# Kernel tuning notes

Hardware: AMD Instinct MI355X
Metric: run time of the kernel (lower is better)

Reference implementation:

```python
import jax, jax.numpy as jnp
import numpy as np

N, M_CODES, Z_DIM = 4096, 4096, 1024


def setup_inputs() -> dict:
    key = jax.random.key(0)
    k1, k2 = jax.random.split(key)
    z = jax.random.normal(k1, (N, Z_DIM), dtype=jnp.float32)
    e = jax.random.normal(k2, (M_CODES, Z_DIM), dtype=jnp.float32)
    return {"z": z, "e": e}


def reference(z, e):
    # Squared pairwise L2 distances [N, M] via GEMM expansion:
    # ||z_i - e_j||^2 = ||z_i||^2 + ||e_j||^2 - 2 z_i . e_j
    z_sq = jnp.sum(z * z, axis=1)               # [N]
    e_sq = jnp.sum(e * e, axis=1)               # [M]
    cross = jnp.einsum('nd,md->nm', z, e)       # [N, M]
    dist = z_sq[:, None] + e_sq[None, :] - 2.0 * cross  # [N, M]
    # min over dim 0 (over data points N) -> per-code nearest distance [M]
    loss = jnp.mean(jnp.min(dist, axis=0))
    return loss
```

## Files before the change

### kernel.cpp

```cpp
#include <hip/hip_runtime.h>
#include <hip/hip_bf16.h>
#include <stdint.h>

#define N_PTS   4096
#define M_CODES 4096
#define ZDIM    1024
#define BM 128
#define BN 128
#define BK 32

typedef __attribute__((ext_vector_type(8))) short bf16x8;
typedef __attribute__((ext_vector_type(4))) float f32x4;

__device__ __forceinline__ unsigned short f2bf(float f) {
    __hip_bfloat16 h = __float2bfloat16(f);
    return *reinterpret_cast<unsigned short*>(&h);
}

__device__ __forceinline__ unsigned enc_f32(float f) {
    unsigned u = __float_as_uint(f);
    return (u & 0x80000000u) ? ~u : (u | 0x80000000u);
}
__device__ __forceinline__ float dec_f32(unsigned e) {
    unsigned u = (e & 0x80000000u) ? (e ^ 0x80000000u) : ~e;
    return __uint_as_float(u);
}

__global__ __launch_bounds__(256) void prep_kernel(
    const float* __restrict__ z, const float* __restrict__ e,
    unsigned short* __restrict__ zb, unsigned short* __restrict__ eb,
    float* __restrict__ zsq, float* __restrict__ esq,
    unsigned* __restrict__ min_enc) {
    const int t = threadIdx.x;
    const int b = blockIdx.x;
    if (b < 16) min_enc[b * 256 + t] = 0xFFFFFFFFu;

    const int w = t >> 6, lane = t & 63;
    const bool is_z = b < 512;
    #pragma unroll
    for (int r2 = 0; r2 < 2; r2++) {
        const int rr = (b & 511) * 8 + w * 2 + r2;
        const float4* s4 =
            reinterpret_cast<const float4*>((is_z ? z : e) + (size_t)rr * ZDIM);
        ushort4* d4 =
            reinterpret_cast<ushort4*>((is_z ? zb : eb) + (size_t)rr * ZDIM);
        float4 v0 = s4[lane], v1 = s4[64 + lane], v2 = s4[128 + lane],
               v3 = s4[192 + lane];
        ushort4 o0, o1, o2, o3;
        o0.x = f2bf(v0.x); o0.y = f2bf(v0.y); o0.z = f2bf(v0.z); o0.w = f2bf(v0.w);
        o1.x = f2bf(v1.x); o1.y = f2bf(v1.y); o1.z = f2bf(v1.z); o1.w = f2bf(v1.w);
        o2.x = f2bf(v2.x); o2.y = f2bf(v2.y); o2.z = f2bf(v2.z); o2.w = f2bf(v2.w);
        o3.x = f2bf(v3.x); o3.y = f2bf(v3.y); o3.z = f2bf(v3.z); o3.w = f2bf(v3.w);
        d4[lane] = o0; d4[64 + lane] = o1; d4[128 + lane] = o2; d4[192 + lane] = o3;
        float s = v0.x * v0.x + v0.y * v0.y + v0.z * v0.z + v0.w * v0.w
                + v1.x * v1.x + v1.y * v1.y + v1.z * v1.z + v1.w * v1.w
                + v2.x * v2.x + v2.y * v2.y + v2.z * v2.z + v2.w * v2.w
                + v3.x * v3.x + v3.y * v3.y + v3.z * v3.z + v3.w * v3.w;
        #pragma unroll
        for (int off = 1; off < 64; off <<= 1) s += __shfl_xor(s, off, 64);
        if (lane == 0) {
            if (is_z) zsq[rr] = s; else esq[rr] = s;
        }
    }
}

__global__ __launch_bounds__(256) void gemm_min_kernel(
    const unsigned short* __restrict__ zb, const unsigned short* __restrict__ eb,
    const float* __restrict__ zsq, unsigned* __restrict__ min_enc) {
    __shared__ __align__(16) unsigned short As[2 * BM * BK];
    __shared__ __align__(16) unsigned short Bs[2 * BN * BK];
    __shared__ float zsq_s[BM];

    const int t = threadIdx.x;
    const int bx = blockIdx.x;
    const int by = blockIdx.y;
    const int lane = t & 63;
    const int w = t >> 6;
    const int wm = w >> 1, wn = w & 1;
    const int lrow = lane & 15;
    const int q = lane >> 4;

    if (t < BM) zsq_s[t] = zsq[by * BM + t];

    f32x4 acc[4][4];
    #pragma unroll
    for (int i = 0; i < 4; i++)
        #pragma unroll
        for (int j = 0; j < 4; j++) acc[i][j] = (f32x4){0.f, 0.f, 0.f, 0.f};

    const int row0 = (t * 16) >> 6;
    const int kel0 = ((t * 16) & 63) >> 1;
    const int lds_b0 = w * 512;
    const size_t a_base = (size_t)(by * BM) * ZDIM;
    const size_t b_base = (size_t)(bx * BN) * ZDIM;

    for (int k0 = 0; k0 < ZDIM; k0 += 2 * BK) {
        #pragma unroll
        for (int s = 0; s < 2; s++) {
            const unsigned short* ga0 =
                zb + a_base + (size_t)row0 * ZDIM + k0 + s * BK + kel0;
            const unsigned short* gb0 =
                eb + b_base + (size_t)row0 * ZDIM + k0 + s * BK + kel0;
            __builtin_amdgcn_global_load_lds(
                (const __attribute__((address_space(1))) void*)ga0,
                (__attribute__((address_space(3))) void*)(As + s * 4096 + lds_b0),
                16, 0, 0);
            __builtin_amdgcn_global_load_lds(
                (const __attribute__((address_space(1))) void*)(ga0 + (size_t)64 * ZDIM),
                (__attribute__((address_space(3))) void*)(As + s * 4096 + 2048 + lds_b0),
                16, 0, 0);
            __builtin_amdgcn_global_load_lds(
                (const __attribute__((address_space(1))) void*)gb0,
                (__attribute__((address_space(3))) void*)(Bs + s * 4096 + lds_b0),
                16, 0, 0);
            __builtin_amdgcn_global_load_lds(
                (const __attribute__((address_space(1))) void*)(gb0 + (size_t)64 * ZDIM),
                (__attribute__((address_space(3))) void*)(Bs + s * 4096 + 2048 + lds_b0),
                16, 0, 0);
        }
        __syncthreads();

        #pragma unroll
        for (int s = 0; s < 2; s++) {
            bf16x8 a[4], bb[4];
            #pragma unroll
            for (int am = 0; am < 4; am++)
                a[am] = *(const bf16x8*)(As + s * 4096 +
                                         (wm * 64 + am * 16 + lrow) * BK + q * 8);
            #pragma unroll
            for (int an = 0; an < 4; an++)
                bb[an] = *(const bf16x8*)(Bs + s * 4096 +
                                          (wn * 64 + an * 16 + lrow) * BK + q * 8);
            #pragma unroll
            for (int am = 0; am < 4; am++)
                #pragma unroll
                for (int an = 0; an < 4; an++)
                    acc[am][an] = __builtin_amdgcn_mfma_f32_16x16x32_bf16(
                        a[am], bb[an], acc[am][an], 0, 0, 0);
        }
        __syncthreads();
    }

    #pragma unroll
    for (int an = 0; an < 4; an++) {
        float v = 3.4e38f;
        #pragma unroll
        for (int am = 0; am < 4; am++) {
            const int rbase = wm * 64 + am * 16 + q * 4;
            f32x4 c = acc[am][an];
            v = fminf(v, zsq_s[rbase + 0] - 2.f * c[0]);
            v = fminf(v, zsq_s[rbase + 1] - 2.f * c[1]);
            v = fminf(v, zsq_s[rbase + 2] - 2.f * c[2]);
            v = fminf(v, zsq_s[rbase + 3] - 2.f * c[3]);
        }
        v = fminf(v, __shfl_xor(v, 16, 64));
        v = fminf(v, __shfl_xor(v, 32, 64));
        if (q == 0) {
            const int col = bx * BN + wn * 64 + an * 16 + lrow;
            atomicMin(&min_enc[col], enc_f32(v));
        }
    }
}

__global__ __launch_bounds__(256) void finalize_kernel(
    const unsigned* __restrict__ min_enc, const float* __restrict__ esq,
    float* __restrict__ out) {
    const int t = threadIdx.x;
    float s = 0.f;
    #pragma unroll
    for (int i = 0; i < M_CODES / 256; i++) {
        const int j = i * 256 + t;
        s += dec_f32(min_enc[j]) + esq[j];
    }
    #pragma unroll
    for (int off = 1; off < 64; off <<= 1) s += __shfl_xor(s, off, 64);
    __shared__ float red[4];
    if ((t & 63) == 0) red[t >> 6] = s;
    __syncthreads();
    if (t == 0) out[0] = (red[0] + red[1] + red[2] + red[3]) * (1.f / M_CODES);
}

extern "C" void kernel_launch(void* const* d_in, const int* in_sizes, int n_in,
                              void* d_out, int out_size, void* d_ws, size_t ws_size,
                              hipStream_t stream) {
    (void)in_sizes; (void)n_in; (void)out_size; (void)ws_size;
    const float* z = (const float*)d_in[0];
    const float* e = (const float*)d_in[1];
    char* ws = (char*)d_ws;
    unsigned short* zb = (unsigned short*)ws;
    unsigned short* eb = (unsigned short*)(ws + ((size_t)8 << 20));
    float* zsq = (float*)(ws + ((size_t)16 << 20));
    float* esq = (float*)(ws + ((size_t)16 << 20) + 16384);
    unsigned* min_enc = (unsigned*)(ws + ((size_t)16 << 20) + 32768);

    prep_kernel<<<dim3(1024), dim3(256), 0, stream>>>(
        z, e, zb, eb, zsq, esq, min_enc);
    gemm_min_kernel<<<dim3(M_CODES / BN, N_PTS / BM), dim3(256), 0, stream>>>(
        zb, eb, zsq, min_enc);
    finalize_kernel<<<dim3(1), dim3(256), 0, stream>>>(min_enc, esq, (float*)d_out);
}
```

Baseline: 117.1 us.

## Pre-swizzle bf16 operands into MFMA fragment layout and use 2-wave 128x128 tiles

The prep kernel now stages 16 rows in LDS and writes the bf16 copies of z and e in a tiled layout, grouped by 16-row panel and 8-element k-group. The GEMM can then fetch each fragment with contiguous lane*8 LDS reads, avoiding strided row access and bank conflicts. The GEMM block shrinks to 128 threads (2 waves), each wave computing 64x128 with 32 accumulators, and loads a 64-wide k slab per iteration. Column minima are combined across waves in LDS before a single atomicMin per column. The trade-off is higher register pressure and fewer waves per block, which may reduce latency hiding.

```diff
diff --git a/kernel.cpp b/kernel.cpp
--- a/kernel.cpp
+++ b/kernel.cpp
@@ -5,9 +5,7 @@
 #define N_PTS   4096
 #define M_CODES 4096
 #define ZDIM    1024
-#define BM 128
-#define BN 128
-#define BK 32
+#define KG      (ZDIM / 8)
 
 typedef __attribute__((ext_vector_type(8))) short bf16x8;
 typedef __attribute__((ext_vector_type(4))) float f32x4;
@@ -16,7 +14,6 @@
     __hip_bfloat16 h = __float2bfloat16(f);
     return *reinterpret_cast<unsigned short*>(&h);
 }
-
 __device__ __forceinline__ unsigned enc_f32(float f) {
     unsigned u = __float_as_uint(f);
     return (u & 0x80000000u) ? ~u : (u | 0x80000000u);
@@ -26,115 +23,109 @@
     return __uint_as_float(u);
 }
 
+#define PREP_PITCH 1032
 __global__ __launch_bounds__(256) void prep_kernel(
     const float* __restrict__ z, const float* __restrict__ e,
     unsigned short* __restrict__ zb, unsigned short* __restrict__ eb,
     float* __restrict__ zsq, float* __restrict__ esq,
     unsigned* __restrict__ min_enc) {
+    __shared__ unsigned short tile[16 * PREP_PITCH];
+    __shared__ float redbuf[16 * 4];
+
     const int t = threadIdx.x;
     const int b = blockIdx.x;
     if (b < 16) min_enc[b * 256 + t] = 0xFFFFFFFFu;
 
+    const bool is_z = b < 256;
+    const int rb = b & 255;
+    const float* src = (is_z ? z : e) + (size_t)rb * 16 * ZDIM;
+    unsigned short* dst = (is_z ? zb : eb) + (size_t)rb * 16384;
     const int w = t >> 6, lane = t & 63;
-    const bool is_z = b < 512;
+
     #pragma unroll
-    for (int r2 = 0; r2 < 2; r2++) {
-        const int rr = (b & 511) * 8 + w * 2 + r2;
-        const float4* s4 =
-            reinterpret_cast<const float4*>((is_z ? z : e) + (size_t)rr * ZDIM);
-        ushort4* d4 =
-            reinterpret_cast<ushort4*>((is_z ? zb : eb) + (size_t)rr * ZDIM);
-        float4 v0 = s4[lane], v1 = s4[64 + lane], v2 = s4[128 + lane],
-               v3 = s4[192 + lane];
-        ushort4 o0, o1, o2, o3;
-        o0.x = f2bf(v0.x); o0.y = f2bf(v0.y); o0.z = f2bf(v0.z); o0.w = f2bf(v0.w);
-        o1.x = f2bf(v1.x); o1.y = f2bf(v1.y); o1.z = f2bf(v1.z); o1.w = f2bf(v1.w);
-        o2.x = f2bf(v2.x); o2.y = f2bf(v2.y); o2.z = f2bf(v2.z); o2.w = f2bf(v2.w);
-        o3.x = f2bf(v3.x); o3.y = f2bf(v3.y); o3.z = f2bf(v3.z); o3.w = f2bf(v3.w);
-        d4[lane] = o0; d4[64 + lane] = o1; d4[128 + lane] = o2; d4[192 + lane] = o3;
-        float s = v0.x * v0.x + v0.y * v0.y + v0.z * v0.z + v0.w * v0.w
-                + v1.x * v1.x + v1.y * v1.y + v1.z * v1.z + v1.w * v1.w
-                + v2.x * v2.x + v2.y * v2.y + v2.z * v2.z + v2.w * v2.w
-                + v3.x * v3.x + v3.y * v3.y + v3.z * v3.z + v3.w * v3.w;
+    for (int it = 0; it < 16; it++) {
+        float4 v = reinterpret_cast<const float4*>(src + (size_t)it * ZDIM)[t];
+        ushort4 o;
+        o.x = f2bf(v.x); o.y = f2bf(v.y); o.z = f2bf(v.z); o.w = f2bf(v.w);
+        *reinterpret_cast<ushort4*>(&tile[it * PREP_PITCH + t * 4]) = o;
+        float s = v.x * v.x + v.y * v.y + v.z * v.z + v.w * v.w;
         #pragma unroll
         for (int off = 1; off < 64; off <<= 1) s += __shfl_xor(s, off, 64);
-        if (lane == 0) {
-            if (is_z) zsq[rr] = s; else esq[rr] = s;
-        }
+        if (lane == 0) redbuf[it * 4 + w] = s;
+    }
+    __syncthreads();
+
+    #pragma unroll
+    for (int it2 = 0; it2 < 8; it2++) {
+        const int c = it2 * 256 + t;
+        const int kg = c >> 4, r16 = c & 15;
+        bf16x8 val = *reinterpret_cast<const bf16x8*>(
+            &tile[r16 * PREP_PITCH + kg * 8]);
+        *reinterpret_cast<bf16x8*>(&dst[(size_t)c * 8]) = val;
+    }
+    if (t < 16) {
+        float sq = redbuf[t * 4] + redbuf[t * 4 + 1] +
+                   redbuf[t * 4 + 2] + redbuf[t * 4 + 3];
+        const int row = rb * 16 + t;
+        if (is_z) zsq[row] = sq; else esq[row] = sq;
     }
 }
 
-__global__ __launch_bounds__(256) void gemm_min_kernel(
+__global__ __launch_bounds__(128) void gemm_min_kernel(
     const unsigned short* __restrict__ zb, const unsigned short* __restrict__ eb,
     const float* __restrict__ zsq, unsigned* __restrict__ min_enc) {
-    __shared__ __align__(16) unsigned short As[2 * BM * BK];
-    __shared__ __align__(16) unsigned short Bs[2 * BN * BK];
-    __shared__ float zsq_s[BM];
+    __shared__ __align__(16) unsigned short As[8192];
+    __shared__ __align__(16) unsigned short Bs[8192];
+    __shared__ float zsq_s[128];
+    __shared__ float colmin[2][128];
 
     const int t = threadIdx.x;
     const int bx = blockIdx.x;
     const int by = blockIdx.y;
     const int lane = t & 63;
     const int w = t >> 6;
-    const int wm = w >> 1, wn = w & 1;
     const int lrow = lane & 15;
     const int q = lane >> 4;
 
-    if (t < BM) zsq_s[t] = zsq[by * BM + t];
+    zsq_s[t] = zsq[by * 128 + t];
 
-    f32x4 acc[4][4];
+    f32x4 acc[4][8];
     #pragma unroll
     for (int i = 0; i < 4; i++)
         #pragma unroll
-        for (int j = 0; j < 4; j++) acc[i][j] = (f32x4){0.f, 0.f, 0.f, 0.f};
+        for (int j = 0; j < 8; j++) acc[i][j] = (f32x4){0.f, 0.f, 0.f, 0.f};
 
-    const int row0 = (t * 16) >> 6;
-    const int kel0 = ((t * 16) & 63) >> 1;
-    const int lds_b0 = w * 512;
-    const size_t a_base = (size_t)(by * BM) * ZDIM;
-    const size_t b_base = (size_t)(bx * BN) * ZDIM;
-
-    for (int k0 = 0; k0 < ZDIM; k0 += 2 * BK) {
+    for (int kg0 = 0; kg0 < KG; kg0 += 8) {
         #pragma unroll
-        for (int s = 0; s < 2; s++) {
-            const unsigned short* ga0 =
-                zb + a_base + (size_t)row0 * ZDIM + k0 + s * BK + kel0;
-            const unsigned short* gb0 =
-                eb + b_base + (size_t)row0 * ZDIM + k0 + s * BK + kel0;
+        for (int j = 0; j < 8; j++) {
+            const unsigned short* ga =
+                zb + (size_t)(by * 8 + j) * 16384 + kg0 * 128 + t * 8;
+            const unsigned short* gb =
+                eb + (size_t)(bx * 8 + j) * 16384 + kg0 * 128 + t * 8;
             __builtin_amdgcn_global_load_lds(
-                (const __attribute__((address_space(1))) void*)ga0,
-                (__attribute__((address_space(3))) void*)(As + s * 4096 + lds_b0),
+                (const __attribute__((address_space(1))) void*)ga,
+                (__attribute__((address_space(3))) void*)(As + j * 1024 + w * 512),
                 16, 0, 0);
             __builtin_amdgcn_global_load_lds(
-                (const __attribute__((address_space(1))) void*)(ga0 + (size_t)64 * ZDIM),
-                (__attribute__((address_space(3))) void*)(As + s * 4096 + 2048 + lds_b0),
-                16, 0, 0);
-            __builtin_amdgcn_global_load_lds(
-                (const __attribute__((address_space(1))) void*)gb0,
-                (__attribute__((address_space(3))) void*)(Bs + s * 4096 + lds_b0),
-                16, 0, 0);
-            __builtin_amdgcn_global_load_lds(
-                (const __attribute__((address_space(1))) void*)(gb0 + (size_t)64 * ZDIM),
-                (__attribute__((address_space(3))) void*)(Bs + s * 4096 + 2048 + lds_b0),
+                (const __attribute__((address_space(1))) void*)gb,
+                (__attribute__((address_space(3))) void*)(Bs + j * 1024 + w * 512),
                 16, 0, 0);
         }
         __syncthreads();
 
         #pragma unroll
         for (int s = 0; s < 2; s++) {
-            bf16x8 a[4], bb[4];
+            bf16x8 a[4], bb[8];
             #pragma unroll
             for (int am = 0; am < 4; am++)
-                a[am] = *(const bf16x8*)(As + s * 4096 +
-                                         (wm * 64 + am * 16 + lrow) * BK + q * 8);
+                a[am] = *(const bf16x8*)(As + (w * 4 + am) * 1024 + s * 512 + lane * 8);
             #pragma unroll
-            for (int an = 0; an < 4; an++)
-                bb[an] = *(const bf16x8*)(Bs + s * 4096 +
-                                          (wn * 64 + an * 16 + lrow) * BK + q * 8);
+            for (int an = 0; an < 8; an++)
+                bb[an] = *(const bf16x8*)(Bs + an * 1024 + s * 512 + lane * 8);
             #pragma unroll
             for (int am = 0; am < 4; am++)
                 #pragma unroll
-                for (int an = 0; an < 4; an++)
+                for (int an = 0; an < 8; an++)
                     acc[am][an] = __builtin_amdgcn_mfma_f32_16x16x32_bf16(
                         a[am], bb[an], acc[am][an], 0, 0, 0);
         }
@@ -142,11 +133,11 @@
     }
 
     #pragma unroll
-    for (int an = 0; an < 4; an++) {
+    for (int an = 0; an < 8; an++) {
         float v = 3.4e38f;
         #pragma unroll
         for (int am = 0; am < 4; am++) {
-            const int rbase = wm * 64 + am * 16 + q * 4;
+            const int rbase = w * 64 + am * 16 + q * 4;
             f32x4 c = acc[am][an];
             v = fminf(v, zsq_s[rbase + 0] - 2.f * c[0]);
             v = fminf(v, zsq_s[rbase + 1] - 2.f * c[1]);
@@ -155,10 +146,12 @@
         }
         v = fminf(v, __shfl_xor(v, 16, 64));
         v = fminf(v, __shfl_xor(v, 32, 64));
-        if (q == 0) {
-            const int col = bx * BN + wn * 64 + an * 16 + lrow;
-            atomicMin(&min_enc[col], enc_f32(v));
-        }
+        if (q == 0) colmin[w][an * 16 + lrow] = v;
+    }
+    __syncthreads();
+    {
+        const float m = fminf(colmin[0][t], colmin[1][t]);
+        atomicMin(&min_enc[bx * 128 + t], enc_f32(m));
     }
 }
 
@@ -193,9 +186,9 @@
     float* esq = (float*)(ws + ((size_t)16 << 20) + 16384);
     unsigned* min_enc = (unsigned*)(ws + ((size_t)16 << 20) + 32768);
 
-    prep_kernel<<<dim3(1024), dim3(256), 0, stream>>>(
+    prep_kernel<<<dim3(512), dim3(256), 0, stream>>>(
         z, e, zb, eb, zsq, esq, min_enc);
-    gemm_min_kernel<<<dim3(M_CODES / BN, N_PTS / BM), dim3(256), 0, stream>>>(
+    gemm_min_kernel<<<dim3(32, 32), dim3(128), 0, stream>>>(
         zb, eb, zsq, min_enc);
     finalize_kernel<<<dim3(1), dim3(256), 0, stream>>>(min_enc, esq, (float*)d_out);
 }
```

Measured after the change: 131.0 us. 11.8% more time.
